# Kernel optimization log

Hardware: AMD Instinct MI355X
Metric: run time of the kernel (lower is better)

Reference implementation:

```python
import jax, jax.numpy as jnp
import numpy as np

B, T, D, H = 2, 2048, 2048, 16
d_head = D // H  # 128


def _rope(x):
    # x: [B, T, H, d]
    d = x.shape[-1]
    inv_freq = 1.0 / (10000.0 ** (jnp.arange(0, d, 2, dtype=jnp.float32) / d))
    t = jnp.arange(x.shape[1], dtype=jnp.float32)
    freqs = t[:, None] * inv_freq[None, :]          # [T, d/2]
    emb = jnp.concatenate([freqs, freqs], axis=-1)  # [T, d]
    cos = jnp.cos(emb)[None, :, None, :]
    sin = jnp.sin(emb)[None, :, None, :]
    x1, x2 = x[..., ::2], x[..., 1::2]
    rot = jnp.stack([-x2, x1], axis=-1).reshape(x.shape)
    return x * cos + rot * sin


def setup_inputs() -> dict:
    key = jax.random.key(0)
    ks = jax.random.split(key, 8)
    s = 1.0 / np.sqrt(D)
    return {
        "x": jax.random.normal(ks[0], (B, T, D), dtype=jnp.float32),
        "W_q": jax.random.normal(ks[1], (D, D), dtype=jnp.float32) * s,
        "W_k": jax.random.normal(ks[2], (D, D), dtype=jnp.float32) * s,
        "W_v": jax.random.normal(ks[3], (D, D), dtype=jnp.float32) * s,
        "W_gate": jax.random.normal(ks[4], (D, D), dtype=jnp.float32) * s,
        "W_p": jax.random.normal(ks[5], (D, D), dtype=jnp.float32) * s,
        "W_clock": jax.random.normal(ks[6], (D, H), dtype=jnp.float32) * s,
        "W_c": jax.random.normal(ks[7], (D, D), dtype=jnp.float32) * s,
    }


def _caps_forward(x, W_q, W_k, W_v, W_gate, W_p, W_clock, W_c):
    Bx, Tx, Dx = x.shape
    q = (x @ W_q).reshape(Bx, Tx, H, d_head)
    k = (x @ W_k).reshape(Bx, Tx, H, d_head)
    v = (x @ W_v).reshape(Bx, Tx, H, d_head)

    clock = jax.nn.softplus(x @ W_clock).reshape(Bx, Tx, H, 1) + 1e-6
    log_clock = jnp.log(clock)

    q = _rope(q)
    k = _rope(k)

    # Branch 1: p_exp normalization
    p = (x @ W_p).reshape(Bx, Tx, H, d_head) + log_clock
    p_max = jnp.max(p, axis=1, keepdims=True)
    p_exp = jnp.exp(p - p_max)
    p_cs = jnp.cumsum(p_exp, axis=1)
    q1 = q / (p_cs + 1e-8)
    k1 = k * p_exp

    # Branch 2: SPD gate cumprod via clipped cumsum
    gj = -jax.nn.softplus(x @ W_gate).reshape(Bx, Tx, H, d_head) * clock
    gj_cp = jnp.exp(jnp.clip(jnp.cumsum(gj, axis=1), -50.0, 40.0))
    q2 = q * gj_cp
    k2 = k / (gj_cp + 1e-8)

    # Branch 3: clock time scaling
    clock_cs = jnp.cumsum(clock, axis=1)
    q3 = q / clock_cs
    k3 = k * clock

    q_cat = jnp.concatenate([q1, q2, q3], axis=-1)  # [B,T,H,3d]
    k_cat = jnp.concatenate([k1, k2, k3], axis=-1)

    scale = 1.0 / jnp.sqrt(jnp.float32(3 * d_head))  # SDPA default: 1/sqrt(q last dim)
    scores = jnp.einsum('bthd,bshd->bhts', q_cat, k_cat) * scale
    attn = jax.nn.softmax(scores, axis=-1)
    out = jnp.einsum('bhts,bshd->bthd', attn, v).reshape(Bx, Tx, Dx)
    return out @ W_c


def reference(x, W_q, W_k, W_v, W_gate, W_p, W_clock, W_c):
    return _caps_forward(x, W_q, W_k, W_v, W_gate, W_p, W_clock, W_c)
```

## Files before the change

kernel.cpp:

```cpp
#include <hip/hip_runtime.h>

typedef unsigned short ushort;
typedef __attribute__((ext_vector_type(8))) short short8;
typedef __attribute__((ext_vector_type(4))) short short4v;
typedef __attribute__((ext_vector_type(4))) float f32x4;

#define Bb 2
#define Tt 2048
#define Dd 2048
#define Hh 16
#define Mm 4096
#define MD 8388608u

__device__ __forceinline__ float b2f(ushort u) {
  union { unsigned int ui; float f; } v; v.ui = ((unsigned int)u) << 16; return v.f;
}
__device__ __forceinline__ ushort f2b(float f) {
  union { float f; unsigned int u; } v; v.f = f;
  unsigned int r = (v.u + 0x7fffu + ((v.u >> 16) & 1u)) >> 16;
  return (ushort)r;
}
__device__ __forceinline__ void split3(float v, ushort& s0, ushort& s1, ushort& s2) {
  ushort a = f2b(v);        float f0 = b2f(a);
  float r1 = v - f0;        ushort b = f2b(r1);  float f1 = b2f(b);
  float r2 = r1 - f1;       ushort c = f2b(r2);
  s0 = a; s1 = b; s2 = c;
}
__device__ __forceinline__ void split3_rtz(float v, ushort& s0, ushort& s1, ushort& s2) {
  union { float f; unsigned u; } c; c.f = v;
  s0 = (ushort)(c.u >> 16);
  union { unsigned u; float f; } h; h.u = c.u & 0xffff0000u;
  float r1 = v - h.f;
  union { float f; unsigned u; } c1; c1.f = r1;
  s1 = (ushort)(c1.u >> 16);
  union { unsigned u; float f; } h1; h1.u = c1.u & 0xffff0000u;
  float r2 = r1 - h1.f;
  s2 = f2b(r2);
}
__device__ __forceinline__ void split2(float v, ushort& s0, ushort& s1) {
  union { float f; unsigned u; } c; c.f = v;
  s0 = (ushort)(c.u >> 16);
  union { unsigned u; float f; } h; h.u = c.u & 0xffff0000u;
  s1 = f2b(v - h.f);
}
__device__ __forceinline__ float softplusf(float x) {
  return fmaxf(x, 0.f) + log1pf(expf(-fabsf(x)));
}
__device__ __forceinline__ short4v tr16(unsigned a) {
  short4v d;
  asm volatile("ds_read_b64_tr_b16 %0, %1" : "=v"(d) : "v"(a));
  return d;
}

__global__ __launch_bounds__(256) void xsplit_k(const float* __restrict__ x,
                                                ushort* __restrict__ S0,
                                                ushort* __restrict__ S1,
                                                ushort* __restrict__ S2) {
  size_t i = ((size_t)blockIdx.x * 256 + threadIdx.x) * 8;
  float v[8];
  *(float4*)&v[0] = *(const float4*)(x + i);
  *(float4*)&v[4] = *(const float4*)(x + i + 4);
  ushort h0[8], h1[8], h2[8];
#pragma unroll
  for (int j = 0; j < 8; ++j) split3_rtz(v[j], h0[j], h1[j], h2[j]);
  *(uint4*)(S0 + i) = *(uint4*)h0;
  *(uint4*)(S1 + i) = *(uint4*)h1;
  *(uint4*)(S2 + i) = *(uint4*)h2;
}

template <int NP>
__global__ __launch_bounds__(256) void split_transposeN(const float* __restrict__ W,
                                                        ushort* __restrict__ T0,
                                                        ushort* __restrict__ T1,
                                                        ushort* __restrict__ T2) {
  __shared__ float tile[64][68];
  int k0 = blockIdx.x << 6, n0 = blockIdx.y << 6;
  int r = threadIdx.x >> 2, c0 = (threadIdx.x & 3) << 4;
  const float* src = W + (size_t)(k0 + r) * Dd + n0 + c0;
#pragma unroll
  for (int q = 0; q < 4; ++q)
    *(float4*)&tile[r][c0 + 4 * q] = *(const float4*)(src + 4 * q);
  __syncthreads();
  ushort h0[16], h1[16], h2[16];
#pragma unroll
  for (int i = 0; i < 16; ++i) {
    float v = tile[c0 + i][r];
    if (NP == 1) {
      h0[i] = f2b(v);
    } else if (NP == 2) {
      ushort a = f2b(v); h0[i] = a; h1[i] = f2b(v - b2f(a));
    } else {
      split3(v, h0[i], h1[i], h2[i]);
    }
  }
  size_t o = (size_t)(n0 + r) * Dd + k0 + c0;
  *(uint4*)(T0 + o) = *(uint4*)&h0[0];  *(uint4*)(T0 + o + 8) = *(uint4*)&h0[8];
  if (NP >= 2) { *(uint4*)(T1 + o) = *(uint4*)&h1[0];  *(uint4*)(T1 + o + 8) = *(uint4*)&h1[8]; }
  if (NP >= 3) { *(uint4*)(T2 + o) = *(uint4*)&h2[0];  *(uint4*)(T2 + o + 8) = *(uint4*)&h2[8]; }
}

template <int BF16OUT>
__global__ __launch_bounds__(256) void gemm63(const float* __restrict__ A,
                                              const ushort* __restrict__ B0,
                                              const ushort* __restrict__ B1,
                                              void* __restrict__ CBase) {
  const int N = 2048, K = 2048;
  int m0 = blockIdx.y << 6, n0 = blockIdx.x << 6;
  __shared__ ushort As0[4096], As1[4096];
  __shared__ ushort Bs0[4096], Bs1[4096];
  int tid = threadIdx.x;
  int row = tid >> 2, c0 = (tid & 3) << 4;
  int sw = row & 7;
  int g0 = c0 >> 3;
  int dst0 = row * 64 + ((g0 ^ sw) << 3);
  int dst1 = row * 64 + (((g0 + 1) ^ sw) << 3);
  const float* aptr = A + (size_t)(m0 + row) * K + c0;
  const ushort* b0p = B0 + (size_t)(n0 + row) * K + c0;
  const ushort* b1p = B1 + (size_t)(n0 + row) * K + c0;
  int lane = tid & 63, wave = tid >> 6;
  int l16 = lane & 15, quad = lane >> 4;
  int wm = (wave & 1) << 5, wn = (wave >> 1) << 5;
  f32x4 acc[2][2] = {};
  for (int k0 = 0; k0 < K; k0 += 64) {
    float av[16];
#pragma unroll
    for (int q = 0; q < 4; ++q)
      *(float4*)&av[4 * q] = *(const float4*)(aptr + k0 + 4 * q);
    ushort a0[16], a1[16];
#pragma unroll
    for (int i = 0; i < 16; ++i) split2(av[i], a0[i], a1[i]);
    uint4 b00 = *(const uint4*)(b0p + k0), b01 = *(const uint4*)(b0p + k0 + 8);
    uint4 b10 = *(const uint4*)(b1p + k0), b11 = *(const uint4*)(b1p + k0 + 8);
    *(uint4*)&As0[dst0] = *(uint4*)&a0[0];  *(uint4*)&As0[dst1] = *(uint4*)&a0[8];
    *(uint4*)&As1[dst0] = *(uint4*)&a1[0];  *(uint4*)&As1[dst1] = *(uint4*)&a1[8];
    *(uint4*)&Bs0[dst0] = b00;  *(uint4*)&Bs0[dst1] = b01;
    *(uint4*)&Bs1[dst0] = b10;  *(uint4*)&Bs1[dst1] = b11;
    __syncthreads();
#pragma unroll
    for (int kk = 0; kk < 2; ++kk) {
      short8 af0[2], af1[2], bf0[2], bf1[2];
#pragma unroll
      for (int mi = 0; mi < 2; ++mi) {
        int rr = wm + (mi << 4) + l16;
        int g = (kk << 2) + quad;
        int idx = rr * 64 + ((g ^ (rr & 7)) << 3);
        af0[mi] = *(const short8*)&As0[idx];
        af1[mi] = *(const short8*)&As1[idx];
      }
#pragma unroll
      for (int nj = 0; nj < 2; ++nj) {
        int rr = wn + (nj << 4) + l16;
        int g = (kk << 2) + quad;
        int idx = rr * 64 + ((g ^ (rr & 7)) << 3);
        bf0[nj] = *(const short8*)&Bs0[idx];
        bf1[nj] = *(const short8*)&Bs1[idx];
      }
#pragma unroll
      for (int mi = 0; mi < 2; ++mi)
#pragma unroll
        for (int nj = 0; nj < 2; ++nj) {
          acc[mi][nj] = __builtin_amdgcn_mfma_f32_16x16x32_bf16(af1[mi], bf0[nj], acc[mi][nj], 0, 0, 0);
          acc[mi][nj] = __builtin_amdgcn_mfma_f32_16x16x32_bf16(af0[mi], bf1[nj], acc[mi][nj], 0, 0, 0);
          acc[mi][nj] = __builtin_amdgcn_mfma_f32_16x16x32_bf16(af0[mi], bf0[nj], acc[mi][nj], 0, 0, 0);
        }
    }
    __syncthreads();
  }
#pragma unroll
  for (int mi = 0; mi < 2; ++mi)
#pragma unroll
    for (int nj = 0; nj < 2; ++nj)
#pragma unroll
      for (int r = 0; r < 4; ++r) {
        int mm = m0 + wm + (mi << 4) + (quad << 2) + r;
        int nn = n0 + wn + (nj << 4) + l16;
        float v = acc[mi][nj][r];
        if (BF16OUT)
          ((ushort*)CBase)[(size_t)mm * N + nn] = f2b(v);
        else
          ((float*)CBase)[(size_t)mm * N + nn] = v;
      }
}

__global__ __launch_bounds__(256) void gemm_pre3(const ushort* __restrict__ A0,
                                                 const ushort* __restrict__ A1,
                                                 const ushort* __restrict__ B0,
                                                 const ushort* __restrict__ B1,
                                                 float* __restrict__ C) {
  const int N = 2048, K = 2048;
  int m0 = blockIdx.y << 6, n0 = blockIdx.x << 6;
  __shared__ ushort As0[4096], As1[4096];
  __shared__ ushort Bs0[4096], Bs1[4096];
  int tid = threadIdx.x;
  int row = tid >> 2, c0 = (tid & 3) << 4;
  int sw = row & 7;
  int g0 = c0 >> 3;
  int dst0 = row * 64 + ((g0 ^ sw) << 3);
  int dst1 = row * 64 + (((g0 + 1) ^ sw) << 3);
  const ushort* a0p = A0 + (size_t)(m0 + row) * K + c0;
  const ushort* a1p = A1 + (size_t)(m0 + row) * K + c0;
  const ushort* b0p = B0 + (size_t)(n0 + row) * K + c0;
  const ushort* b1p = B1 + (size_t)(n0 + row) * K + c0;
  int lane = tid & 63, wave = tid >> 6;
  int l16 = lane & 15, quad = lane >> 4;
  int wm = (wave & 1) << 5, wn = (wave >> 1) << 5;
  f32x4 acc[2][2] = {};
  for (int k0 = 0; k0 < K; k0 += 64) {
    uint4 a00 = *(const uint4*)(a0p + k0), a01 = *(const uint4*)(a0p + k0 + 8);
    uint4 a10 = *(const uint4*)(a1p + k0), a11 = *(const uint4*)(a1p + k0 + 8);
    uint4 b00 = *(const uint4*)(b0p + k0), b01 = *(const uint4*)(b0p + k0 + 8);
    uint4 b10 = *(const uint4*)(b1p + k0), b11 = *(const uint4*)(b1p + k0 + 8);
    *(uint4*)&As0[dst0] = a00;  *(uint4*)&As0[dst1] = a01;
    *(uint4*)&As1[dst0] = a10;  *(uint4*)&As1[dst1] = a11;
    *(uint4*)&Bs0[dst0] = b00;  *(uint4*)&Bs0[dst1] = b01;
    *(uint4*)&Bs1[dst0] = b10;  *(uint4*)&Bs1[dst1] = b11;
    __syncthreads();
#pragma unroll
    for (int kk = 0; kk < 2; ++kk) {
      short8 af0[2], af1[2], bf0[2], bf1[2];
#pragma unroll
      for (int mi = 0; mi < 2; ++mi) {
        int rr = wm + (mi << 4) + l16;
        int g = (kk << 2) + quad;
        int idx = rr * 64 + ((g ^ (rr & 7)) << 3);
        af0[mi] = *(const short8*)&As0[idx];
        af1[mi] = *(const short8*)&As1[idx];
      }
#pragma unroll
      for (int nj = 0; nj < 2; ++nj) {
        int rr = wn + (nj << 4) + l16;
        int g = (kk << 2) + quad;
        int idx = rr * 64 + ((g ^ (rr & 7)) << 3);
        bf0[nj] = *(const short8*)&Bs0[idx];
        bf1[nj] = *(const short8*)&Bs1[idx];
      }
#pragma unroll
      for (int mi = 0; mi < 2; ++mi)
#pragma unroll
        for (int nj = 0; nj < 2; ++nj) {
          acc[mi][nj] = __builtin_amdgcn_mfma_f32_16x16x32_bf16(af1[mi], bf0[nj], acc[mi][nj], 0, 0, 0);
          acc[mi][nj] = __builtin_amdgcn_mfma_f32_16x16x32_bf16(af0[mi], bf1[nj], acc[mi][nj], 0, 0, 0);
          acc[mi][nj] = __builtin_amdgcn_mfma_f32_16x16x32_bf16(af0[mi], bf0[nj], acc[mi][nj], 0, 0, 0);
        }
    }
    __syncthreads();
  }
#pragma unroll
  for (int mi = 0; mi < 2; ++mi)
#pragma unroll
    for (int nj = 0; nj < 2; ++nj)
#pragma unroll
      for (int r = 0; r < 4; ++r) {
        int mm = m0 + wm + (mi << 4) + (quad << 2) + r;
        int nn = n0 + wn + (nj << 4) + l16;
        C[(size_t)mm * N + nn] = acc[mi][nj][r];
      }
}

__global__ __launch_bounds__(256) void gemm_pre(const ushort* __restrict__ A0,
                                                const ushort* __restrict__ A1,
                                                const ushort* __restrict__ A2,
                                                const ushort* __restrict__ B0,
                                                const ushort* __restrict__ B1,
                                                const ushort* __restrict__ B2,
                                                float* __restrict__ C) {
  const int N = 2048, K = 2048;
  int m0 = blockIdx.y << 6, n0 = blockIdx.x << 6;
  __shared__ ushort As0[4096], As1[4096], As2[4096];
  __shared__ ushort Bs0[4096], Bs1[4096], Bs2[4096];
  int tid = threadIdx.x;
  int row = tid >> 2, c0 = (tid & 3) << 4;
  int sw = row & 7;
  int g0 = c0 >> 3;
  int dst0 = row * 64 + ((g0 ^ sw) << 3);
  int dst1 = row * 64 + (((g0 + 1) ^ sw) << 3);
  const ushort* a0p = A0 + (size_t)(m0 + row) * K + c0;
  const ushort* a1p = A1 + (size_t)(m0 + row) * K + c0;
  const ushort* a2p = A2 + (size_t)(m0 + row) * K + c0;
  const ushort* b0p = B0 + (size_t)(n0 + row) * K + c0;
  const ushort* b1p = B1 + (size_t)(n0 + row) * K + c0;
  const ushort* b2p = B2 + (size_t)(n0 + row) * K + c0;
  int lane = tid & 63, wave = tid >> 6;
  int l16 = lane & 15, quad = lane >> 4;
  int wm = (wave & 1) << 5, wn = (wave >> 1) << 5;
  f32x4 acc[2][2] = {};
  for (int k0 = 0; k0 < K; k0 += 64) {
    uint4 a00 = *(const uint4*)(a0p + k0), a01 = *(const uint4*)(a0p + k0 + 8);
    uint4 a10 = *(const uint4*)(a1p + k0), a11 = *(const uint4*)(a1p + k0 + 8);
    uint4 a20 = *(const uint4*)(a2p + k0), a21 = *(const uint4*)(a2p + k0 + 8);
    uint4 b00 = *(const uint4*)(b0p + k0), b01 = *(const uint4*)(b0p + k0 + 8);
    uint4 b10 = *(const uint4*)(b1p + k0), b11 = *(const uint4*)(b1p + k0 + 8);
    uint4 b20 = *(const uint4*)(b2p + k0), b21 = *(const uint4*)(b2p + k0 + 8);
    *(uint4*)&As0[dst0] = a00;  *(uint4*)&As0[dst1] = a01;
    *(uint4*)&As1[dst0] = a10;  *(uint4*)&As1[dst1] = a11;
    *(uint4*)&As2[dst0] = a20;  *(uint4*)&As2[dst1] = a21;
    *(uint4*)&Bs0[dst0] = b00;  *(uint4*)&Bs0[dst1] = b01;
    *(uint4*)&Bs1[dst0] = b10;  *(uint4*)&Bs1[dst1] = b11;
    *(uint4*)&Bs2[dst0] = b20;  *(uint4*)&Bs2[dst1] = b21;
    __syncthreads();
#pragma unroll
    for (int kk = 0; kk < 2; ++kk) {
      short8 af0[2], af1[2], af2[2], bf0[2], bf1[2], bf2[2];
#pragma unroll
      for (int mi = 0; mi < 2; ++mi) {
        int rr = wm + (mi << 4) + l16;
        int g = (kk << 2) + quad;
        int idx = rr * 64 + ((g ^ (rr & 7)) << 3);
        af0[mi] = *(const short8*)&As0[idx];
        af1[mi] = *(const short8*)&As1[idx];
        af2[mi] = *(const short8*)&As2[idx];
      }
#pragma unroll
      for (int nj = 0; nj < 2; ++nj) {
        int rr = wn + (nj << 4) + l16;
        int g = (kk << 2) + quad;
        int idx = rr * 64 + ((g ^ (rr & 7)) << 3);
        bf0[nj] = *(const short8*)&Bs0[idx];
        bf1[nj] = *(const short8*)&Bs1[idx];
        bf2[nj] = *(const short8*)&Bs2[idx];
      }
#pragma unroll
      for (int mi = 0; mi < 2; ++mi)
#pragma unroll
        for (int nj = 0; nj < 2; ++nj) {
          acc[mi][nj] = __builtin_amdgcn_mfma_f32_16x16x32_bf16(af2[mi], bf0[nj], acc[mi][nj], 0, 0, 0);
          acc[mi][nj] = __builtin_amdgcn_mfma_f32_16x16x32_bf16(af0[mi], bf2[nj], acc[mi][nj], 0, 0, 0);
          acc[mi][nj] = __builtin_amdgcn_mfma_f32_16x16x32_bf16(af1[mi], bf1[nj], acc[mi][nj], 0, 0, 0);
          acc[mi][nj] = __builtin_amdgcn_mfma_f32_16x16x32_bf16(af1[mi], bf0[nj], acc[mi][nj], 0, 0, 0);
          acc[mi][nj] = __builtin_amdgcn_mfma_f32_16x16x32_bf16(af0[mi], bf1[nj], acc[mi][nj], 0, 0, 0);
          acc[mi][nj] = __builtin_amdgcn_mfma_f32_16x16x32_bf16(af0[mi], bf0[nj], acc[mi][nj], 0, 0, 0);
        }
    }
    __syncthreads();
  }
#pragma unroll
  for (int mi = 0; mi < 2; ++mi)
#pragma unroll
    for (int nj = 0; nj < 2; ++nj)
#pragma unroll
      for (int r = 0; r < 4; ++r) {
        int mm = m0 + wm + (mi << 4) + (quad << 2) + r;
        int nn = n0 + wn + (nj << 4) + l16;
        C[(size_t)mm * N + nn] = acc[mi][nj][r];
      }
}

__global__ __launch_bounds__(256) void gemm_b16A(const ushort* __restrict__ A,
                                                 const ushort* __restrict__ Bt,
                                                 float* __restrict__ C) {
  const int N = 2048, K = 2048;
  int m0 = blockIdx.y << 6, n0 = blockIdx.x << 6;
  __shared__ ushort As[64 * 64];
  __shared__ ushort Bs[64 * 64];
  int tid = threadIdx.x;
  int row = tid >> 2, c0 = (tid & 3) << 4;
  int sw = row & 7;
  int g0 = c0 >> 3;
  int dst0 = row * 64 + ((g0 ^ sw) << 3);
  int dst1 = row * 64 + (((g0 + 1) ^ sw) << 3);
  const ushort* aptr = A + (size_t)(m0 + row) * K + c0;
  const ushort* bptr = Bt + (size_t)(n0 + row) * K + c0;
  int lane = tid & 63, wave = tid >> 6;
  int l16 = lane & 15, quad = lane >> 4;
  int wm = (wave & 1) << 5, wn = (wave >> 1) << 5;
  f32x4 acc[2][2] = {};
  for (int k0 = 0; k0 < K; k0 += 64) {
    uint4 av0 = *(const uint4*)(aptr + k0);
    uint4 av1 = *(const uint4*)(aptr + k0 + 8);
    uint4 bv0 = *(const uint4*)(bptr + k0);
    uint4 bv1 = *(const uint4*)(bptr + k0 + 8);
    *(uint4*)&As[dst0] = av0;
    *(uint4*)&As[dst1] = av1;
    *(uint4*)&Bs[dst0] = bv0;
    *(uint4*)&Bs[dst1] = bv1;
    __syncthreads();
#pragma unroll
    for (int kk = 0; kk < 2; ++kk) {
      short8 af[2], bf[2];
#pragma unroll
      for (int mi = 0; mi < 2; ++mi) {
        int rr = wm + (mi << 4) + l16;
        int g = (kk << 2) + quad;
        af[mi] = *(const short8*)&As[rr * 64 + ((g ^ (rr & 7)) << 3)];
      }
#pragma unroll
      for (int nj = 0; nj < 2; ++nj) {
        int rr = wn + (nj << 4) + l16;
        int g = (kk << 2) + quad;
        bf[nj] = *(const short8*)&Bs[rr * 64 + ((g ^ (rr & 7)) << 3)];
      }
#pragma unroll
      for (int mi = 0; mi < 2; ++mi)
#pragma unroll
        for (int nj = 0; nj < 2; ++nj)
          acc[mi][nj] = __builtin_amdgcn_mfma_f32_16x16x32_bf16(af[mi], bf[nj], acc[mi][nj], 0, 0, 0);
    }
    __syncthreads();
  }
#pragma unroll
  for (int mi = 0; mi < 2; ++mi)
#pragma unroll
    for (int nj = 0; nj < 2; ++nj)
#pragma unroll
      for (int r = 0; r < 4; ++r) {
        int mm = m0 + wm + (mi << 4) + (quad << 2) + r;
        int nn = n0 + wn + (nj << 4) + l16;
        C[(size_t)mm * N + nn] = acc[mi][nj][r];
      }
}

__global__ __launch_bounds__(64) void wclock_k(const float* __restrict__ x,
                                               const float* __restrict__ Wc,
                                               float* __restrict__ out) {
  int m = blockIdx.x, lane = threadIdx.x;
  const float* xr = x + (size_t)m * Dd;
  float acc[16];
#pragma unroll
  for (int h = 0; h < 16; ++h) acc[h] = 0.f;
  for (int k = lane; k < Dd; k += 64) {
    float xv = xr[k];
    const float* wr = Wc + k * 16;
#pragma unroll
    for (int h = 0; h < 16; ++h) acc[h] += xv * wr[h];
  }
#pragma unroll
  for (int h = 0; h < 16; ++h) {
#pragma unroll
    for (int off = 32; off; off >>= 1) acc[h] += __shfl_down(acc[h], off);
  }
  if (lane == 0) {
    float* o = out + (size_t)m * 16;
#pragma unroll
    for (int h = 0; h < 16; ++h) o[h] = acc[h];
  }
}

__global__ __launch_bounds__(128) void pmaxchunk_k(const float* __restrict__ Pf,
                                                   const float* __restrict__ cpre,
                                                   float* __restrict__ pmaxc) {
  int bh = blockIdx.x, ch = blockIdx.y, d = threadIdx.x;
  int b = bh >> 4, h = bh & 15;
  float mx = -1e30f;
  int t0 = ch << 8;
  for (int t = t0; t < t0 + 256; ++t) {
    float pr = Pf[((size_t)(b * Tt + t)) * Dd + h * 128 + d];
    float c = softplusf(cpre[(b * Tt + t) * Hh + h]) + 1e-6f;
    mx = fmaxf(mx, pr + logf(c));
  }
  pmaxc[(size_t)(bh * 8 + ch) * 128 + d] = mx;
}

__global__ __launch_bounds__(128) void scan_ew_k(float* planes,
                                                 const float* __restrict__ cpre,
                                                 const float* __restrict__ pmaxc,
                                                 float* __restrict__ clockv,
                                                 float* __restrict__ sum_pe,
                                                 float* __restrict__ sum_gj,
                                                 float* __restrict__ sum_ck) {
  int ch = blockIdx.x, bh = blockIdx.y;
  int b = bh >> 4, h = bh & 15, d = threadIdx.x;
  float* Qf = planes;
  float* Kf = planes + (size_t)MD;
  float* Gf = planes + 2 * (size_t)MD;
  float* Pf = planes + 3 * (size_t)MD;
  float invf = (float)exp(-((double)((d & 63) * 2) / 128.0) * log(10000.0));
  float pmax = -1e30f;
#pragma unroll
  for (int c = 0; c < 8; ++c) pmax = fmaxf(pmax, pmaxc[(size_t)(bh * 8 + c) * 128 + d]);
  float s_pe = 0.f, s_gj = 0.f, s_ck = 0.f;
  int t0 = ch << 5;
#pragma unroll 4
  for (int i = 0; i < 32; ++i) {
    int t = t0 + i;
    size_t off = ((size_t)(b * Tt + t)) * Dd + h * 128 + d;
    float qv = Qf[off], kv = Kf[off], pv = Pf[off], gv = Gf[off];
    float clock = softplusf(cpre[(b * Tt + t) * Hh + h]) + 1e-6f;
    float ang = (float)t * invf;
    float c_ = cosf(ang), s_ = sinf(ang);
    float qp = __shfl_xor(qv, 1);
    float kp = __shfl_xor(kv, 1);
    float qrot = (d & 1) ? qp : -qp;
    float krot = (d & 1) ? kp : -kp;
    float qr = qv * c_ + qrot * s_;
    float kr = kv * c_ + krot * s_;
    float pe = expf(pv + logf(clock) - pmax);
    s_pe += pe;
    float gj = -softplusf(gv) * clock;
    s_gj += gj;
    Qf[off] = qr;
    Kf[off] = kr;
    Gf[off] = gj;
    Pf[off] = pe;
    if (d == 0) {
      clockv[bh * Tt + t] = clock;
      s_ck += clock;
    }
  }
  size_t so = (size_t)(bh * 64 + ch) * 128 + d;
  sum_pe[so] = s_pe;
  sum_gj[so] = s_gj;
  if (d == 0) sum_ck[bh * 64 + ch] = s_ck;
}

__global__ __launch_bounds__(128) void scan_off_k(const float* __restrict__ sum_pe,
                                                  const float* __restrict__ sum_gj,
                                                  const float* __restrict__ sum_ck,
                                                  float* __restrict__ pcs_cp,
                                                  float* __restrict__ goff,
                                                  float* __restrict__ coff) {
  int bh = blockIdx.x, d = threadIdx.x;
  float ppe = 0.f, pgj = 0.f, pck = 0.f;
  for (int c = 0; c < 64; ++c) {
    size_t o = (size_t)(bh * 64 + c) * 128 + d;
    pcs_cp[o] = ppe;
    goff[o] = pgj;
    ppe += sum_pe[o];
    pgj += sum_gj[o];
    if (d == 0) { coff[bh * 64 + c] = pck; pck += sum_ck[bh * 64 + c]; }
  }
}

__global__ __launch_bounds__(128) void scan_apply_k(float* planes,
                                                    const float* __restrict__ goff,
                                                    const float* __restrict__ coff,
                                                    const float* __restrict__ clockv,
                                                    float* __restrict__ ccsv) {
  int ch = blockIdx.x, bh = blockIdx.y;
  int b = bh >> 4, h = bh & 15, d = threadIdx.x;
  float* Gf = planes + 2 * (size_t)MD;
  float g = goff[(size_t)(bh * 64 + ch) * 128 + d];
  float ccs = (d == 0) ? coff[bh * 64 + ch] : 0.f;
  int t0 = ch << 5;
#pragma unroll 4
  for (int i = 0; i < 32; ++i) {
    int t = t0 + i;
    size_t off = ((size_t)(b * Tt + t)) * Dd + h * 128 + d;
    float gj = Gf[off];
    g += gj;
    float e = expf(fminf(fmaxf(g, -50.f), 40.f));
    Gf[off] = e;
    if (d == 0) {
      ccs += clockv[bh * Tt + t];
      ccsv[bh * Tt + t] = ccs;
    }
  }
}

__global__ __launch_bounds__(512, 2) void attn_mfma_k(const float* __restrict__ planes,
                                                      const ushort* __restrict__ Vb,
                                                      const float* __restrict__ clockv,
                                                      const float* __restrict__ ccsv,
                                                      const float* __restrict__ pcs_cp,
                                                      ushort* __restrict__ attnout) {
  __shared__ float smemf[18432];
  ushort* Khi = (ushort*)smemf;
  ushort* Klo = Khi + 12288;
  ushort* Vsm = Khi + 24576;
  unsigned* Pu = (unsigned*)(smemf + 14336);
  float* pcsL = smemf;
  ushort* qscr = (ushort*)(smemf + 8192);

  int tid = threadIdx.x;
  int lane = tid & 63, wave = tid >> 6;
  int l15 = lane & 15, qd = lane >> 4;
  int qt0 = blockIdx.x << 7;
  int bh = blockIdx.y, b = bh >> 4, h = bh & 15;
  const float* Qf = planes;
  const float* Kf = planes + (size_t)MD;
  const float* Ef = planes + 2 * (size_t)MD;
  const float* Pe = planes + 3 * (size_t)MD;
  size_t pbase = ((size_t)b * Tt) * Dd + h * 128;

  short8 qh[12], ql[12];
  int wl = wave & 3;
  int rloc = lane >> 2;
  {
    ushort* sh = qscr + (wl << 12);
    ushort* sl = sh + 2048;
#pragma unroll
    for (int rd = 0; rd < 2; ++rd) {
      if (tid < 256) {
        int d = tid & 127, seg = tid >> 7;
        int rbase = (rd << 6) + (seg << 5);
        float pcs = pcs_cp[((size_t)bh * 64 + (qt0 >> 5) + (rd << 1) + seg) * 128 + d];
        for (int i = 0; i < 32; ++i) {
          pcs += Pe[pbase + (size_t)(qt0 + rbase + i) * Dd + d];
          pcsL[((seg << 5) + i) * 128 + d] = pcs;
        }
      }
      __syncthreads();
      int part = ((wave >> 2) == rd);
      int grow = qt0 + (rd << 6) + (wl << 4) + rloc;
      float ccsr = __builtin_amdgcn_rcpf(ccsv[bh * Tt + grow]);
      size_t goffq = pbase + (size_t)grow * Dd;
#pragma unroll
      for (int cd = 0; cd < 3; ++cd) {
        __syncthreads();
        if (part) {
#pragma unroll
          for (int j = 0; j < 4; ++j) {
            int d0 = ((lane & 3) << 5) + (j << 3);
            float qv[8], mv[8];
            *(float4*)&qv[0] = *(const float4*)(Qf + goffq + d0);
            *(float4*)&qv[4] = *(const float4*)(Qf + goffq + d0 + 4);
            if (cd == 0) {
              *(float4*)&mv[0] = *(const float4*)&pcsL[((wl << 4) + rloc) * 128 + d0];
              *(float4*)&mv[4] = *(const float4*)&pcsL[((wl << 4) + rloc) * 128 + d0 + 4];
#pragma unroll
              for (int i = 0; i < 8; ++i) qv[i] = qv[i] * __builtin_amdgcn_rcpf(mv[i] + 1e-8f);
            } else if (cd == 1) {
              *(float4*)&mv[0] = *(const float4*)(Ef + goffq + d0);
              *(float4*)&mv[4] = *(const float4*)(Ef + goffq + d0 + 4);
#pragma unroll
              for (int i = 0; i < 8; ++i) qv[i] = qv[i] * mv[i];
            } else {
#pragma unroll
              for (int i = 0; i < 8; ++i) qv[i] = qv[i] * ccsr;
            }
            ushort hi8[8], lo8[8];
#pragma unroll
            for (int i = 0; i < 8; ++i) {
              ushort a = f2b(qv[i]); hi8[i] = a; lo8[i] = f2b(qv[i] - b2f(a));
            }
            int g = ((lane & 3) << 2) + j;
            int phys = (g & 8) | ((g ^ rloc) & 7);
            *(uint4*)&sh[rloc * 128 + (phys << 3)] = *(uint4*)hi8;
            *(uint4*)&sl[rloc * 128 + (phys << 3)] = *(uint4*)lo8;
          }
        }
        __syncthreads();
        if (part) {
#pragma unroll
          for (int ksl = 0; ksl < 4; ++ksl) {
            int g = (ksl << 2) + qd;
            int phys = (g & 8) | ((g ^ l15) & 7);
            qh[(cd << 2) + ksl] = *(const short8*)&sh[l15 * 128 + (phys << 3)];
            ql[(cd << 2) + ksl] = *(const short8*)&sl[l15 * 128 + (phys << 3)];
          }
        }
      }
      __syncthreads();
    }
  }

  float mi4[4], li4[4];
  f32x4 acc_pv[8] = {};
#pragma unroll
  for (int r = 0; r < 4; ++r) { mi4[r] = -1e30f; li4[r] = 0.f; }
  const float scl = 0.05103103630798287f;
  const ushort* vbase = Vb + pbase;
  unsigned* PuW = Pu + (wave << 9);
  unsigned VsmA = (unsigned)(size_t)Vsm;
  int kk = tid >> 4;
  int kdb = tid & 15;

  for (int st = 0; st < 64; ++st) {
    int s0 = st << 5;
    __syncthreads();
    {
      size_t roff = pbase + (size_t)(s0 + kk) * Dd + (kdb << 3);
      float ck = clockv[bh * Tt + s0 + kk];
      float kv[8], pev[8], ev[8];
      *(float4*)&kv[0] = *(const float4*)(Kf + roff);
      *(float4*)&kv[4] = *(const float4*)(Kf + roff + 4);
      *(float4*)&pev[0] = *(const float4*)(Pe + roff);
      *(float4*)&pev[4] = *(const float4*)(Pe + roff + 4);
      *(float4*)&ev[0] = *(const float4*)(Ef + roff);
      *(float4*)&ev[4] = *(const float4*)(Ef + roff + 4);
#pragma unroll
      for (int slot = 0; slot < 3; ++slot) {
        float val[8];
        if (slot == 0) {
#pragma unroll
          for (int i = 0; i < 8; ++i) val[i] = kv[i] * pev[i];
        } else if (slot == 1) {
#pragma unroll
          for (int i = 0; i < 8; ++i) val[i] = kv[i] * __builtin_amdgcn_rcpf(ev[i] + 1e-8f);
        } else {
#pragma unroll
          for (int i = 0; i < 8; ++i) val[i] = kv[i] * ck;
        }
        unsigned ub[8], ul[8];
#pragma unroll
        for (int i = 0; i < 8; ++i) {
          union { float f; unsigned u; } c; c.f = val[i];
          ub[i] = c.u;
          union { unsigned u; float f; } hm; hm.u = c.u & 0xffff0000u;
          union { float f; unsigned u; } lr; lr.f = val[i] - hm.f;
          ul[i] = lr.u;
        }
        uint4 hi4, lo4;
        hi4.x = (ub[0] >> 16) | (ub[1] & 0xffff0000u);
        hi4.y = (ub[2] >> 16) | (ub[3] & 0xffff0000u);
        hi4.z = (ub[4] >> 16) | (ub[5] & 0xffff0000u);
        hi4.w = (ub[6] >> 16) | (ub[7] & 0xffff0000u);
        lo4.x = (ul[0] >> 16) | (ul[1] & 0xffff0000u);
        lo4.y = (ul[2] >> 16) | (ul[3] & 0xffff0000u);
        lo4.z = (ul[4] >> 16) | (ul[5] & 0xffff0000u);
        lo4.w = (ul[6] >> 16) | (ul[7] & 0xffff0000u);
        int g = (slot << 4) + kdb;
        int phys = (g & ~7) | ((g ^ kk) & 7);
        *(uint4*)&Khi[kk * 384 + (phys << 3)] = hi4;
        *(uint4*)&Klo[kk * 384 + (phys << 3)] = lo4;
      }
      const ushort* vsrc = vbase + (size_t)(s0 + kk) * Dd + (kdb << 3);
      int vbyte = ((kdb >> 1) << 10) + (((kk >> 2) & 1) << 9) + ((kk >> 3) << 7) +
                  ((kk & 3) << 5) + ((kdb & 1) << 4);
      *(uint4*)((char*)Vsm + vbyte) = *(const uint4*)vsrc;
    }
    __syncthreads();
    f32x4 acc0 = {}, acc1 = {};
#pragma unroll
    for (int ks = 0; ks < 12; ++ks) {
      int g = (ks << 2) + qd;
      int p0i = (g & ~7) | ((g ^ l15) & 7);
      int p1i = (g & ~7) | ((g ^ (16 + l15)) & 7);
      short8 b0h = *(const short8*)&Khi[l15 * 384 + (p0i << 3)];
      short8 b0l = *(const short8*)&Klo[l15 * 384 + (p0i << 3)];
      short8 b1h = *(const short8*)&Khi[(16 + l15) * 384 + (p1i << 3)];
      short8 b1l = *(const short8*)&Klo[(16 + l15) * 384 + (p1i << 3)];
      acc0 = __builtin_amdgcn_mfma_f32_16x16x32_bf16(ql[ks], b0h, acc0, 0, 0, 0);
      acc0 = __builtin_amdgcn_mfma_f32_16x16x32_bf16(qh[ks], b0l, acc0, 0, 0, 0);
      acc0 = __builtin_amdgcn_mfma_f32_16x16x32_bf16(qh[ks], b0h, acc0, 0, 0, 0);
      acc1 = __builtin_amdgcn_mfma_f32_16x16x32_bf16(ql[ks], b1h, acc1, 0, 0, 0);
      acc1 = __builtin_amdgcn_mfma_f32_16x16x32_bf16(qh[ks], b1l, acc1, 0, 0, 0);
      acc1 = __builtin_amdgcn_mfma_f32_16x16x32_bf16(qh[ks], b1h, acc1, 0, 0, 0);
    }
#pragma unroll
    for (int r = 0; r < 4; ++r) {
      float sa = acc0[r] * scl, sb = acc1[r] * scl;
      float mx = fmaxf(sa, sb);
#pragma unroll
      for (int m = 1; m < 16; m <<= 1) mx = fmaxf(mx, __shfl_xor(mx, m));
      float mn = fmaxf(mi4[r], mx);
      float al = expf(mi4[r] - mn);
      float p0 = expf(sa - mn), p1 = expf(sb - mn);
      float rs = p0 + p1;
#pragma unroll
      for (int m = 1; m < 16; m <<= 1) rs += __shfl_xor(rs, m);
      li4[r] = li4[r] * al + rs;
      mi4[r] = mn;
#pragma unroll
      for (int n0 = 0; n0 < 8; ++n0) acc_pv[n0][r] *= al;
      int R = (qd << 2) + r;
      {
        union { float f; unsigned u; } c0, c1; c0.f = p0; c1.f = p1;
        union { unsigned u; float f; } m0_, m1_;
        m0_.u = c0.u & 0xffff0000u; m1_.u = c1.u & 0xffff0000u;
        union { float f; unsigned u; } d0_, d1_;
        d0_.f = p0 - m0_.f; d1_.f = p1 - m1_.f;
        unsigned u0 = (c0.u >> 16) | (d0_.u & 0xffff0000u);
        unsigned u1 = (c1.u >> 16) | (d1_.u & 0xffff0000u);
        int r7 = R & 7;
        char* pb = (char*)PuW + (R << 7) + ((l15 & 3) << 2);
        *(unsigned*)(pb + (((l15 >> 2) ^ r7) << 4)) = u0;
        *(unsigned*)(pb + ((((l15 >> 2) + 4) ^ r7) << 4)) = u1;
      }
    }
    {
      unsigned pw[8];
      {
        const char* pb = (const char*)PuW + l15 * 128;
        uint4 w0 = *(const uint4*)(pb + ((((qd << 1)) ^ (l15 & 7)) << 4));
        uint4 w1 = *(const uint4*)(pb + ((((qd << 1) | 1) ^ (l15 & 7)) << 4));
        pw[0] = w0.x; pw[1] = w0.y; pw[2] = w0.z; pw[3] = w0.w;
        pw[4] = w1.x; pw[5] = w1.y; pw[6] = w1.z; pw[7] = w1.w;
      }
      union { unsigned u[4]; short8 s; } uph, upl;
#pragma unroll
      for (int i = 0; i < 4; ++i) {
        uph.u[i] = (pw[2 * i] & 0xffffu) | (pw[2 * i + 1] << 16);
        upl.u[i] = (pw[2 * i] >> 16) | (pw[2 * i + 1] & 0xffff0000u);
      }
      short4v tv[16];
#pragma unroll
      for (int n0 = 0; n0 < 8; ++n0) {
        unsigned a0 = VsmA + (n0 << 10) + (lane << 3);
        tv[2 * n0] = tr16(a0);
        tv[2 * n0 + 1] = tr16(a0 + 512);
      }
      asm volatile("s_waitcnt lgkmcnt(0)" ::: "memory");
      __builtin_amdgcn_sched_barrier(0);
#pragma unroll
      for (int n0 = 0; n0 < 8; ++n0) {
        short8 bv = __builtin_shufflevector(tv[2 * n0], tv[2 * n0 + 1], 0, 1, 2, 3, 4, 5, 6, 7);
        acc_pv[n0] = __builtin_amdgcn_mfma_f32_16x16x32_bf16(uph.s, bv, acc_pv[n0], 0, 0, 0);
        acc_pv[n0] = __builtin_amdgcn_mfma_f32_16x16x32_bf16(upl.s, bv, acc_pv[n0], 0, 0, 0);
      }
    }
  }
#pragma unroll
  for (int r = 0; r < 4; ++r) {
    float inv = 1.f / li4[r];
    int trow = qt0 + (wave << 4) + (qd << 2) + r;
    ushort* orow = attnout + ((size_t)(b * Tt + trow)) * Dd + h * 128 + l15;
#pragma unroll
    for (int n0 = 0; n0 < 8; ++n0)
      orow[n0 << 4] = f2b(acc_pv[n0][r] * inv);
  }
}

extern "C" void kernel_launch(void* const* d_in, const int* in_sizes, int n_in,
                              void* d_out, int out_size, void* d_ws, size_t ws_size,
                              hipStream_t stream) {
  const float* x = (const float*)d_in[0];
  const float* Wq = (const float*)d_in[1];
  const float* Wk = (const float*)d_in[2];
  const float* Wv = (const float*)d_in[3];
  const float* Wg = (const float*)d_in[4];
  const float* Wp = (const float*)d_in[5];
  const float* Wclk = (const float*)d_in[6];
  const float* Wc = (const float*)d_in[7];

  float* planes = (float*)d_ws;
  float* Aq = planes;
  float* Bk = planes + (size_t)MD;
  float* Ce = planes + 2 * (size_t)MD;
  float* Dp = planes + 3 * (size_t)MD;
  ushort* Vb = (ushort*)(planes + 4 * (size_t)MD);
  float* cpre = (float*)(Vb + (size_t)MD);
  float* clockv = cpre + 65536;
  float* ccsv = clockv + 65536;
  float* pmaxc = ccsv + 65536;
  float* pcs_cp = pmaxc + 32768;
  ushort* Wt0 = (ushort*)(pcs_cp + 262144);
  ushort* Wt1 = Wt0 + (size_t)Dd * Dd;
  ushort* Wt2 = Wt1 + (size_t)Dd * Dd;
  ushort* attnout = Wt0;
  ushort* WcT0 = (ushort*)Ce;
  ushort* xs0 = (ushort*)Dp;
  ushort* xs1 = xs0 + (size_t)MD;
  ushort* xs2 = (ushort*)Vb;
  float* sum_pe = (float*)Wt2;
  float* sum_gj = sum_pe + 262144;
  float* goff_  = sum_gj + 262144;
  float* sum_ck = goff_ + 262144;
  float* coff_  = sum_ck + 2048;

  size_t needed = (size_t)((char*)(Wt2 + (size_t)Dd * Dd) - (char*)d_ws);
  if (ws_size < needed) return;

  dim3 tg(Dd / 64, Dd / 64), gg(Dd / 64, Mm / 64);

  xsplit_k<<<dim3(MD / 8 / 256), 256, 0, stream>>>(x, xs0, xs1, xs2);

  split_transposeN<2><<<tg, 256, 0, stream>>>(Wq, Wt0, Wt1, nullptr);
  gemm_pre3<<<gg, 256, 0, stream>>>(xs0, xs1, Wt0, Wt1, Aq);
  split_transposeN<2><<<tg, 256, 0, stream>>>(Wk, Wt0, Wt1, nullptr);
  gemm_pre3<<<gg, 256, 0, stream>>>(xs0, xs1, Wt0, Wt1, Bk);
  split_transposeN<3><<<tg, 256, 0, stream>>>(Wg, Wt0, Wt1, Wt2);
  gemm_pre<<<gg, 256, 0, stream>>>(xs0, xs1, xs2, Wt0, Wt1, Wt2, Ce);
  split_transposeN<2><<<tg, 256, 0, stream>>>(Wp, Wt0, Wt1, nullptr);
  gemm63<0><<<gg, 256, 0, stream>>>(x, Wt0, Wt1, (void*)Dp);
  split_transposeN<2><<<tg, 256, 0, stream>>>(Wv, Wt0, Wt1, nullptr);
  gemm63<1><<<gg, 256, 0, stream>>>(x, Wt0, Wt1, (void*)Vb);

  wclock_k<<<dim3(Mm), dim3(64), 0, stream>>>(x, Wclk, cpre);
  pmaxchunk_k<<<dim3(Bb * Hh, 8), dim3(128), 0, stream>>>(Dp, cpre, pmaxc);

  scan_ew_k<<<dim3(64, Bb * Hh), dim3(128), 0, stream>>>(planes, cpre, pmaxc, clockv,
                                                         sum_pe, sum_gj, sum_ck);
  scan_off_k<<<dim3(Bb * Hh), dim3(128), 0, stream>>>(sum_pe, sum_gj, sum_ck,
                                                      pcs_cp, goff_, coff_);
  scan_apply_k<<<dim3(64, Bb * Hh), dim3(128), 0, stream>>>(planes, goff_, coff_, clockv, ccsv);

  attn_mfma_k<<<dim3(Tt / 128, Bb * Hh), dim3(512), 0, stream>>>(planes, Vb, clockv, ccsv, pcs_cp, attnout);

  split_transposeN<1><<<tg, 256, 0, stream>>>(Wc, WcT0, nullptr, nullptr);
  gemm_b16A<<<gg, 256, 0, stream>>>(attnout, WcT0, (float*)d_out);
}
```

Before: 1.878 ms.

## Enlarge projection GEMM tiles to 128x128 with 512-thread blocks

Replaces the 64x64-tile split-bf16 GEMM kernels used for the Q, K, P, V and output projections with 128x128-tile versions. Each block now runs 8 waves, and each wave computes a 64x32 sub-tile with more MFMA accumulators. The larger tiles raise data reuse per shared-memory load and cut global traffic for the A and B operands. In exchange they use 64KB of LDS and more registers per block, which lowers occupancy, and launch fewer blocks.

```diff
diff --git a/kernel.cpp b/kernel.cpp
--- a/kernel.cpp
+++ b/kernel.cpp
@@ -99,102 +99,17 @@
   if (NP >= 3) { *(uint4*)(T2 + o) = *(uint4*)&h2[0];  *(uint4*)(T2 + o + 8) = *(uint4*)&h2[8]; }
 }
 
-template <int BF16OUT>
-__global__ __launch_bounds__(256) void gemm63(const float* __restrict__ A,
-                                              const ushort* __restrict__ B0,
-                                              const ushort* __restrict__ B1,
-                                              void* __restrict__ CBase) {
+__global__ __launch_bounds__(512) void gemm128_pre2(const ushort* __restrict__ A0,
+                                                    const ushort* __restrict__ A1,
+                                                    const ushort* __restrict__ B0,
+                                                    const ushort* __restrict__ B1,
+                                                    float* __restrict__ C) {
   const int N = 2048, K = 2048;
-  int m0 = blockIdx.y << 6, n0 = blockIdx.x << 6;
-  __shared__ ushort As0[4096], As1[4096];
-  __shared__ ushort Bs0[4096], Bs1[4096];
+  int m0 = blockIdx.y << 7, n0 = blockIdx.x << 7;
+  __shared__ ushort As0[8192], As1[8192], Bs0[8192], Bs1[8192];
   int tid = threadIdx.x;
   int row = tid >> 2, c0 = (tid & 3) << 4;
-  int sw = row & 7;
-  int g0 = c0 >> 3;
-  int dst0 = row * 64 + ((g0 ^ sw) << 3);
-  int dst1 = row * 64 + (((g0 + 1) ^ sw) << 3);
-  const float* aptr = A + (size_t)(m0 + row) * K + c0;
-  const ushort* b0p = B0 + (size_t)(n0 + row) * K + c0;
-  const ushort* b1p = B1 + (size_t)(n0 + row) * K + c0;
-  int lane = tid & 63, wave = tid >> 6;
-  int l16 = lane & 15, quad = lane >> 4;
-  int wm = (wave & 1) << 5, wn = (wave >> 1) << 5;
-  f32x4 acc[2][2] = {};
-  for (int k0 = 0; k0 < K; k0 += 64) {
-    float av[16];
-#pragma unroll
-    for (int q = 0; q < 4; ++q)
-      *(float4*)&av[4 * q] = *(const float4*)(aptr + k0 + 4 * q);
-    ushort a0[16], a1[16];
-#pragma unroll
-    for (int i = 0; i < 16; ++i) split2(av[i], a0[i], a1[i]);
-    uint4 b00 = *(const uint4*)(b0p + k0), b01 = *(const uint4*)(b0p + k0 + 8);
-    uint4 b10 = *(const uint4*)(b1p + k0), b11 = *(const uint4*)(b1p + k0 + 8);
-    *(uint4*)&As0[dst0] = *(uint4*)&a0[0];  *(uint4*)&As0[dst1] = *(uint4*)&a0[8];
-    *(uint4*)&As1[dst0] = *(uint4*)&a1[0];  *(uint4*)&As1[dst1] = *(uint4*)&a1[8];
-    *(uint4*)&Bs0[dst0] = b00;  *(uint4*)&Bs0[dst1] = b01;
-    *(uint4*)&Bs1[dst0] = b10;  *(uint4*)&Bs1[dst1] = b11;
-    __syncthreads();
-#pragma unroll
-    for (int kk = 0; kk < 2; ++kk) {
-      short8 af0[2], af1[2], bf0[2], bf1[2];
-#pragma unroll
-      for (int mi = 0; mi < 2; ++mi) {
-        int rr = wm + (mi << 4) + l16;
-        int g = (kk << 2) + quad;
-        int idx = rr * 64 + ((g ^ (rr & 7)) << 3);
-        af0[mi] = *(const short8*)&As0[idx];
-        af1[mi] = *(const short8*)&As1[idx];
-      }
-#pragma unroll
-      for (int nj = 0; nj < 2; ++nj) {
-        int rr = wn + (nj << 4) + l16;
-        int g = (kk << 2) + quad;
-        int idx = rr * 64 + ((g ^ (rr & 7)) << 3);
-        bf0[nj] = *(const short8*)&Bs0[idx];
-        bf1[nj] = *(const short8*)&Bs1[idx];
-      }
-#pragma unroll
-      for (int mi = 0; mi < 2; ++mi)
-#pragma unroll
-        for (int nj = 0; nj < 2; ++nj) {
-          acc[mi][nj] = __builtin_amdgcn_mfma_f32_16x16x32_bf16(af1[mi], bf0[nj], acc[mi][nj], 0, 0, 0);
-          acc[mi][nj] = __builtin_amdgcn_mfma_f32_16x16x32_bf16(af0[mi], bf1[nj], acc[mi][nj], 0, 0, 0);
-          acc[mi][nj] = __builtin_amdgcn_mfma_f32_16x16x32_bf16(af0[mi], bf0[nj], acc[mi][nj], 0, 0, 0);
-        }
-    }
-    __syncthreads();
-  }
-#pragma unroll
-  for (int mi = 0; mi < 2; ++mi)
-#pragma unroll
-    for (int nj = 0; nj < 2; ++nj)
-#pragma unroll
-      for (int r = 0; r < 4; ++r) {
-        int mm = m0 + wm + (mi << 4) + (quad << 2) + r;
-        int nn = n0 + wn + (nj << 4) + l16;
-        float v = acc[mi][nj][r];
-        if (BF16OUT)
-          ((ushort*)CBase)[(size_t)mm * N + nn] = f2b(v);
-        else
-          ((float*)CBase)[(size_t)mm * N + nn] = v;
-      }
-}
-
-__global__ __launch_bounds__(256) void gemm_pre3(const ushort* __restrict__ A0,
-                                                 const ushort* __restrict__ A1,
-                                                 const ushort* __restrict__ B0,
-                                                 const ushort* __restrict__ B1,
-                                                 float* __restrict__ C) {
-  const int N = 2048, K = 2048;
-  int m0 = blockIdx.y << 6, n0 = blockIdx.x << 6;
-  __shared__ ushort As0[4096], As1[4096];
-  __shared__ ushort Bs0[4096], Bs1[4096];
-  int tid = threadIdx.x;
-  int row = tid >> 2, c0 = (tid & 3) << 4;
-  int sw = row & 7;
-  int g0 = c0 >> 3;
+  int sw = row & 7, g0 = c0 >> 3;
   int dst0 = row * 64 + ((g0 ^ sw) << 3);
   int dst1 = row * 64 + (((g0 + 1) ^ sw) << 3);
   const ushort* a0p = A0 + (size_t)(m0 + row) * K + c0;
@@ -203,8 +118,8 @@
   const ushort* b1p = B1 + (size_t)(n0 + row) * K + c0;
   int lane = tid & 63, wave = tid >> 6;
   int l16 = lane & 15, quad = lane >> 4;
-  int wm = (wave & 1) << 5, wn = (wave >> 1) << 5;
-  f32x4 acc[2][2] = {};
+  int wm = (wave & 1) << 6, wn = (wave >> 1) << 5;
+  f32x4 acc[4][2] = {};
   for (int k0 = 0; k0 < K; k0 += 64) {
     uint4 a00 = *(const uint4*)(a0p + k0), a01 = *(const uint4*)(a0p + k0 + 8);
     uint4 a10 = *(const uint4*)(a1p + k0), a11 = *(const uint4*)(a1p + k0 + 8);
@@ -217,9 +132,9 @@
     __syncthreads();
 #pragma unroll
     for (int kk = 0; kk < 2; ++kk) {
-      short8 af0[2], af1[2], bf0[2], bf1[2];
-#pragma unroll
-      for (int mi = 0; mi < 2; ++mi) {
+      short8 af0[4], af1[4], bf0[2], bf1[2];
+#pragma unroll
+      for (int mi = 0; mi < 4; ++mi) {
         int rr = wm + (mi << 4) + l16;
         int g = (kk << 2) + quad;
         int idx = rr * 64 + ((g ^ (rr & 7)) << 3);
@@ -235,7 +150,7 @@
         bf1[nj] = *(const short8*)&Bs1[idx];
       }
 #pragma unroll
-      for (int mi = 0; mi < 2; ++mi)
+      for (int mi = 0; mi < 4; ++mi)
 #pragma unroll
         for (int nj = 0; nj < 2; ++nj) {
           acc[mi][nj] = __builtin_amdgcn_mfma_f32_16x16x32_bf16(af1[mi], bf0[nj], acc[mi][nj], 0, 0, 0);
@@ -246,7 +161,146 @@
     __syncthreads();
   }
 #pragma unroll
-  for (int mi = 0; mi < 2; ++mi)
+  for (int mi = 0; mi < 4; ++mi)
+#pragma unroll
+    for (int nj = 0; nj < 2; ++nj)
+#pragma unroll
+      for (int r = 0; r < 4; ++r) {
+        int mm = m0 + wm + (mi << 4) + (quad << 2) + r;
+        int nn = n0 + wn + (nj << 4) + l16;
+        C[(size_t)mm * N + nn] = acc[mi][nj][r];
+      }
+}
+
+template <int BF16OUT>
+__global__ __launch_bounds__(512) void gemm128_split2(const float* __restrict__ A,
+                                                      const ushort* __restrict__ B0,
+                                                      const ushort* __restrict__ B1,
+                                                      void* __restrict__ CBase) {
+  const int N = 2048, K = 2048;
+  int m0 = blockIdx.y << 7, n0 = blockIdx.x << 7;
+  __shared__ ushort As0[8192], As1[8192], Bs0[8192], Bs1[8192];
+  int tid = threadIdx.x;
+  int row = tid >> 2, c0 = (tid & 3) << 4;
+  int sw = row & 7, g0 = c0 >> 3;
+  int dst0 = row * 64 + ((g0 ^ sw) << 3);
+  int dst1 = row * 64 + (((g0 + 1) ^ sw) << 3);
+  const float* aptr = A + (size_t)(m0 + row) * K + c0;
+  const ushort* b0p = B0 + (size_t)(n0 + row) * K + c0;
+  const ushort* b1p = B1 + (size_t)(n0 + row) * K + c0;
+  int lane = tid & 63, wave = tid >> 6;
+  int l16 = lane & 15, quad = lane >> 4;
+  int wm = (wave & 1) << 6, wn = (wave >> 1) << 5;
+  f32x4 acc[4][2] = {};
+  for (int k0 = 0; k0 < K; k0 += 64) {
+    float av[16];
+#pragma unroll
+    for (int q = 0; q < 4; ++q)
+      *(float4*)&av[4 * q] = *(const float4*)(aptr + k0 + 4 * q);
+    ushort a0[16], a1[16];
+#pragma unroll
+    for (int i = 0; i < 16; ++i) split2(av[i], a0[i], a1[i]);
+    uint4 b00 = *(const uint4*)(b0p + k0), b01 = *(const uint4*)(b0p + k0 + 8);
+    uint4 b10 = *(const uint4*)(b1p + k0), b11 = *(const uint4*)(b1p + k0 + 8);
+    *(uint4*)&As0[dst0] = *(uint4*)&a0[0];  *(uint4*)&As0[dst1] = *(uint4*)&a0[8];
+    *(uint4*)&As1[dst0] = *(uint4*)&a1[0];  *(uint4*)&As1[dst1] = *(uint4*)&a1[8];
+    *(uint4*)&Bs0[dst0] = b00;  *(uint4*)&Bs0[dst1] = b01;
+    *(uint4*)&Bs1[dst0] = b10;  *(uint4*)&Bs1[dst1] = b11;
+    __syncthreads();
+#pragma unroll
+    for (int kk = 0; kk < 2; ++kk) {
+      short8 af0[4], af1[4], bf0[2], bf1[2];
+#pragma unroll
+      for (int mi = 0; mi < 4; ++mi) {
+        int rr = wm + (mi << 4) + l16;
+        int g = (kk << 2) + quad;
+        int idx = rr * 64 + ((g ^ (rr & 7)) << 3);
+        af0[mi] = *(const short8*)&As0[idx];
+        af1[mi] = *(const short8*)&As1[idx];
+      }
+#pragma unroll
+      for (int nj = 0; nj < 2; ++nj) {
+        int rr = wn + (nj << 4) + l16;
+        int g = (kk << 2) + quad;
+        int idx = rr * 64 + ((g ^ (rr & 7)) << 3);
+        bf0[nj] = *(const short8*)&Bs0[idx];
+        bf1[nj] = *(const short8*)&Bs1[idx];
+      }
+#pragma unroll
+      for (int mi = 0; mi < 4; ++mi)
+#pragma unroll
+        for (int nj = 0; nj < 2; ++nj) {
+          acc[mi][nj] = __builtin_amdgcn_mfma_f32_16x16x32_bf16(af1[mi], bf0[nj], acc[mi][nj], 0, 0, 0);
+          acc[mi][nj] = __builtin_amdgcn_mfma_f32_16x16x32_bf16(af0[mi], bf1[nj], acc[mi][nj], 0, 0, 0);
+          acc[mi][nj] = __builtin_amdgcn_mfma_f32_16x16x32_bf16(af0[mi], bf0[nj], acc[mi][nj], 0, 0, 0);
+        }
+    }
+    __syncthreads();
+  }
+#pragma unroll
+  for (int mi = 0; mi < 4; ++mi)
+#pragma unroll
+    for (int nj = 0; nj < 2; ++nj)
+#pragma unroll
+      for (int r = 0; r < 4; ++r) {
+        int mm = m0 + wm + (mi << 4) + (quad << 2) + r;
+        int nn = n0 + wn + (nj << 4) + l16;
+        float v = acc[mi][nj][r];
+        if (BF16OUT)
+          ((ushort*)CBase)[(size_t)mm * N + nn] = f2b(v);
+        else
+          ((float*)CBase)[(size_t)mm * N + nn] = v;
+      }
+}
+
+__global__ __launch_bounds__(512) void gemm128_b16(const ushort* __restrict__ A,
+                                                   const ushort* __restrict__ Bt,
+                                                   float* __restrict__ C) {
+  const int N = 2048, K = 2048;
+  int m0 = blockIdx.y << 7, n0 = blockIdx.x << 7;
+  __shared__ ushort As[8192], Bs[8192];
+  int tid = threadIdx.x;
+  int row = tid >> 2, c0 = (tid & 3) << 4;
+  int sw = row & 7, g0 = c0 >> 3;
+  int dst0 = row * 64 + ((g0 ^ sw) << 3);
+  int dst1 = row * 64 + (((g0 + 1) ^ sw) << 3);
+  const ushort* aptr = A + (size_t)(m0 + row) * K + c0;
+  const ushort* bptr = Bt + (size_t)(n0 + row) * K + c0;
+  int lane = tid & 63, wave = tid >> 6;
+  int l16 = lane & 15, quad = lane >> 4;
+  int wm = (wave & 1) << 6, wn = (wave >> 1) << 5;
+  f32x4 acc[4][2] = {};
+  for (int k0 = 0; k0 < K; k0 += 64) {
+    uint4 av0 = *(const uint4*)(aptr + k0), av1 = *(const uint4*)(aptr + k0 + 8);
+    uint4 bv0 = *(const uint4*)(bptr + k0), bv1 = *(const uint4*)(bptr + k0 + 8);
+    *(uint4*)&As[dst0] = av0;  *(uint4*)&As[dst1] = av1;
+    *(uint4*)&Bs[dst0] = bv0;  *(uint4*)&Bs[dst1] = bv1;
+    __syncthreads();
+#pragma unroll
+    for (int kk = 0; kk < 2; ++kk) {
+      short8 af[4], bf[2];
+#pragma unroll
+      for (int mi = 0; mi < 4; ++mi) {
+        int rr = wm + (mi << 4) + l16;
+        int g = (kk << 2) + quad;
+        af[mi] = *(const short8*)&As[rr * 64 + ((g ^ (rr & 7)) << 3)];
+      }
+#pragma unroll
+      for (int nj = 0; nj < 2; ++nj) {
+        int rr = wn + (nj << 4) + l16;
+        int g = (kk << 2) + quad;
+        bf[nj] = *(const short8*)&Bs[rr * 64 + ((g ^ (rr & 7)) << 3)];
+      }
+#pragma unroll
+      for (int mi = 0; mi < 4; ++mi)
+#pragma unroll
+        for (int nj = 0; nj < 2; ++nj)
+          acc[mi][nj] = __builtin_amdgcn_mfma_f32_16x16x32_bf16(af[mi], bf[nj], acc[mi][nj], 0, 0, 0);
+    }
+    __syncthreads();
+  }
+#pragma unroll
+  for (int mi = 0; mi < 4; ++mi)
 #pragma unroll
     for (int nj = 0; nj < 2; ++nj)
 #pragma unroll
@@ -345,70 +399,6 @@
       }
 }
 
-__global__ __launch_bounds__(256) void gemm_b16A(const ushort* __restrict__ A,
-                                                 const ushort* __restrict__ Bt,
-                                                 float* __restrict__ C) {
-  const int N = 2048, K = 2048;
-  int m0 = blockIdx.y << 6, n0 = blockIdx.x << 6;
-  __shared__ ushort As[64 * 64];
-  __shared__ ushort Bs[64 * 64];
-  int tid = threadIdx.x;
-  int row = tid >> 2, c0 = (tid & 3) << 4;
-  int sw = row & 7;
-  int g0 = c0 >> 3;
-  int dst0 = row * 64 + ((g0 ^ sw) << 3);
-  int dst1 = row * 64 + (((g0 + 1) ^ sw) << 3);
-  const ushort* aptr = A + (size_t)(m0 + row) * K + c0;
-  const ushort* bptr = Bt + (size_t)(n0 + row) * K + c0;
-  int lane = tid & 63, wave = tid >> 6;
-  int l16 = lane & 15, quad = lane >> 4;
-  int wm = (wave & 1) << 5, wn = (wave >> 1) << 5;
-  f32x4 acc[2][2] = {};
-  for (int k0 = 0; k0 < K; k0 += 64) {
-    uint4 av0 = *(const uint4*)(aptr + k0);
-    uint4 av1 = *(const uint4*)(aptr + k0 + 8);
-    uint4 bv0 = *(const uint4*)(bptr + k0);
-    uint4 bv1 = *(const uint4*)(bptr + k0 + 8);
-    *(uint4*)&As[dst0] = av0;
-    *(uint4*)&As[dst1] = av1;
-    *(uint4*)&Bs[dst0] = bv0;
-    *(uint4*)&Bs[dst1] = bv1;
-    __syncthreads();
-#pragma unroll
-    for (int kk = 0; kk < 2; ++kk) {
-      short8 af[2], bf[2];
-#pragma unroll
-      for (int mi = 0; mi < 2; ++mi) {
-        int rr = wm + (mi << 4) + l16;
-        int g = (kk << 2) + quad;
-        af[mi] = *(const short8*)&As[rr * 64 + ((g ^ (rr & 7)) << 3)];
-      }
-#pragma unroll
-      for (int nj = 0; nj < 2; ++nj) {
-        int rr = wn + (nj << 4) + l16;
-        int g = (kk << 2) + quad;
-        bf[nj] = *(const short8*)&Bs[rr * 64 + ((g ^ (rr & 7)) << 3)];
-      }
-#pragma unroll
-      for (int mi = 0; mi < 2; ++mi)
-#pragma unroll
-        for (int nj = 0; nj < 2; ++nj)
-          acc[mi][nj] = __builtin_amdgcn_mfma_f32_16x16x32_bf16(af[mi], bf[nj], acc[mi][nj], 0, 0, 0);
-    }
-    __syncthreads();
-  }
-#pragma unroll
-  for (int mi = 0; mi < 2; ++mi)
-#pragma unroll
-    for (int nj = 0; nj < 2; ++nj)
-#pragma unroll
-      for (int r = 0; r < 4; ++r) {
-        int mm = m0 + wm + (mi << 4) + (quad << 2) + r;
-        int nn = n0 + wn + (nj << 4) + l16;
-        C[(size_t)mm * N + nn] = acc[mi][nj][r];
-      }
-}
-
 __global__ __launch_bounds__(64) void wclock_k(const float* __restrict__ x,
                                                const float* __restrict__ Wc,
                                                float* __restrict__ out) {
@@ -840,20 +830,21 @@
   size_t needed = (size_t)((char*)(Wt2 + (size_t)Dd * Dd) - (char*)d_ws);
   if (ws_size < needed) return;
 
-  dim3 tg(Dd / 64, Dd / 64), gg(Dd / 64, Mm / 64);
+  dim3 tg(Dd / 64, Dd / 64);
+  dim3 g128(Dd / 128, Mm / 128), gg(Dd / 64, Mm / 64);
 
   xsplit_k<<<dim3(MD / 8 / 256), 256, 0, stream>>>(x, xs0, xs1, xs2);
 
   split_transposeN<2><<<tg, 256, 0, stream>>>(Wq, Wt0, Wt1, nullptr);
-  gemm_pre3<<<gg, 256, 0, stream>>>(xs0, xs1, Wt0, Wt1, Aq);
+  gemm128_pre2<<<g128, 512, 0, stream>>>(xs0, xs1, Wt0, Wt1, Aq);
   split_transposeN<2><<<tg, 256, 0, stream>>>(Wk, Wt0, Wt1, nullptr);
-  gemm_pre3<<<gg, 256, 0, stream>>>(xs0, xs1, Wt0, Wt1, Bk);
+  gemm128_pre2<<<g128, 512, 0, stream>>>(xs0, xs1, Wt0, Wt1, Bk);
   split_transposeN<3><<<tg, 256, 0, stream>>>(Wg, Wt0, Wt1, Wt2);
   gemm_pre<<<gg, 256, 0, stream>>>(xs0, xs1, xs2, Wt0, Wt1, Wt2, Ce);
   split_transposeN<2><<<tg, 256, 0, stream>>>(Wp, Wt0, Wt1, nullptr);
-  gemm63<0><<<gg, 256, 0, stream>>>(x, Wt0, Wt1, (void*)Dp);
+  gemm128_split2<0><<<g128, 512, 0, stream>>>(x, Wt0, Wt1, (void*)Dp);
   split_transposeN<2><<<tg, 256, 0, stream>>>(Wv, Wt0, Wt1, nullptr);
-  gemm63<1><<<gg, 256, 0, stream>>>(x, Wt0, Wt1, (void*)Vb);
+  gemm128_split2<1><<<g128, 512, 0, stream>>>(x, Wt0, Wt1, (void*)Vb);
 
   wclock_k<<<dim3(Mm), dim3(64), 0, stream>>>(x, Wclk, cpre);
   pmaxchunk_k<<<dim3(Bb * Hh, 8), dim3(128), 0, stream>>>(Dp, cpre, pmaxc);
@@ -867,5 +858,5 @@
   attn_mfma_k<<<dim3(Tt / 128, Bb * Hh), dim3(512), 0, stream>>>(planes, Vb, clockv, ccsv, pcs_cp, attnout);
 
   split_transposeN<1><<<tg, 256, 0, stream>>>(Wc, WcT0, nullptr, nullptr);
-  gemm_b16A<<<gg, 256, 0, stream>>>(attnout, WcT0, (float*)d_out);
-}
+  gemm128_b16<<<g128, 512, 0, stream>>>(attnout, WcT0, (float*)d_out);
+}
```

Result: faster. 1.712 ms (-8.8%).
